# Performance work log

Hardware: AMD Instinct MI355X
Metric: run time of the kernel (lower is better)

Reference implementation:

```python
import jax, jax.numpy as jnp
import numpy as np

B, S, D = 2, 2048, 2048
H = 16
HD = D // H
FF = 8192
EPS = 1e-5


def _layer_norm(x, g, b):
    mu = jnp.mean(x, axis=-1, keepdims=True)
    var = jnp.mean(jnp.square(x - mu), axis=-1, keepdims=True)
    return (x - mu) * jax.lax.rsqrt(var + EPS) * g + b


def setup_inputs() -> dict:
    key = jax.random.key(0)
    ks = jax.random.split(key, 8)
    s = 0.02
    return {
        "x": jax.random.normal(ks[0], (B, S, D), dtype=jnp.float32),
        "ln1_g": jnp.ones((D,), jnp.float32),
        "ln1_b": jnp.zeros((D,), jnp.float32),
        "qkv_w": jax.random.normal(ks[1], (D, 3 * D), dtype=jnp.float32) * s,
        "qkv_b": jnp.zeros((3 * D,), jnp.float32),
        "out_w": jax.random.normal(ks[2], (D, D), dtype=jnp.float32) * s,
        "out_b": jnp.zeros((D,), jnp.float32),
        "ln2_g": jnp.ones((D,), jnp.float32),
        "ln2_b": jnp.zeros((D,), jnp.float32),
        "w1": jax.random.normal(ks[3], (D, FF), dtype=jnp.float32) * s,
        "b1": jnp.zeros((FF,), jnp.float32),
        "w2": jax.random.normal(ks[4], (FF, D), dtype=jnp.float32) * s,
        "b2": jnp.zeros((D,), jnp.float32),
    }


def reference(x, ln1_g, ln1_b, qkv_w, qkv_b, out_w, out_b, ln2_g, ln2_b, w1, b1, w2, b2):
    # --- attention sub-block (pre-norm) ---
    residual = x
    h = _layer_norm(x, ln1_g, ln1_b)
    qkv = h @ qkv_w + qkv_b                      # [B,S,3D]
    q, k, v = jnp.split(qkv, 3, axis=-1)
    # [B,S,D] -> [B,H,S,HD]
    q = q.reshape(B, S, H, HD).transpose(0, 2, 1, 3)
    k = k.reshape(B, S, H, HD).transpose(0, 2, 1, 3)
    v = v.reshape(B, S, H, HD).transpose(0, 2, 1, 3)
    scores = jnp.einsum("bhqd,bhkd->bhqk", q, k)  # [B,H,S,S]
    causal = jnp.triu(jnp.ones((S, S), dtype=bool), k=1)
    scores = jnp.where(causal[None, None], -jnp.inf, scores)
    attn = jax.nn.softmax(scores / np.sqrt(HD).astype(np.float32), axis=-1)
    av = jnp.einsum("bhqk,bhkd->bhqd", attn, v)   # [B,H,S,HD]
    av = av.transpose(0, 2, 1, 3).reshape(B, S, D)
    x = residual + (av @ out_w + out_b)
    # --- FFN sub-block (pre-norm) ---
    residual = x
    h = _layer_norm(x, ln2_g, ln2_b)
    h = jax.nn.gelu(h @ w1 + b1, approximate=False)
    x = residual + (h @ w2 + b2)
    return x
```

## Files before the change

### kernel.cpp

```cpp
#include <hip/hip_runtime.h>
#include <hip/hip_bf16.h>

#define B_  2
#define S_  2048
#define D_  2048
#define H_  16
#define HD_ 128
#define FF_ 8192

typedef __bf16 bf16x8 __attribute__((ext_vector_type(8)));
typedef float  f32x4  __attribute__((ext_vector_type(4)));
typedef unsigned short u16;
typedef u16 u16x8 __attribute__((ext_vector_type(8)));

__device__ __forceinline__ u16 f2bf(float f) {
    union { float f; unsigned u; } c; c.f = f;
    unsigned u = c.u;
    u += 0x7fffu + ((u >> 16) & 1u);
    return (u16)(u >> 16);
}

__device__ __forceinline__ void gld16(void* lds, const void* g) {
    __builtin_amdgcn_global_load_lds(
        (const __attribute__((address_space(1))) unsigned int*)g,
        (__attribute__((address_space(3))) unsigned int*)lds,
        16, 0, 0);
}

__global__ __launch_bounds__(256)
void ln_kernel(const float* __restrict__ x, const float* __restrict__ g,
               const float* __restrict__ bb, u16* __restrict__ out)
{
    int row = blockIdx.x, tid = threadIdx.x;
    const float4* xr = (const float4*)(x + (size_t)row * D_);
    float4 a = xr[tid], c = xr[tid + 256];
    float s  = a.x + a.y + a.z + a.w + c.x + c.y + c.z + c.w;
    float s2 = a.x*a.x + a.y*a.y + a.z*a.z + a.w*a.w
             + c.x*c.x + c.y*c.y + c.z*c.z + c.w*c.w;
    #pragma unroll
    for (int off = 32; off > 0; off >>= 1) {
        s  += __shfl_down(s,  off, 64);
        s2 += __shfl_down(s2, off, 64);
    }
    __shared__ float red[16];
    __shared__ float mr[2];
    int wid = tid >> 6, lane = tid & 63;
    if (lane == 0) { red[wid] = s; red[8 + wid] = s2; }
    __syncthreads();
    if (tid == 0) {
        float ts = red[0] + red[1] + red[2] + red[3];
        float t2 = red[8] + red[9] + red[10] + red[11];
        float mu = ts * (1.0f / D_);
        float var = t2 * (1.0f / D_) - mu * mu;
        mr[0] = mu; mr[1] = rsqrtf(var + 1e-5f);
    }
    __syncthreads();
    float mu = mr[0], rstd = mr[1];
    const float4* gg = (const float4*)g;
    const float4* bv = (const float4*)bb;
    float4 g0 = gg[tid], g1 = gg[tid + 256];
    float4 b0 = bv[tid], b1 = bv[tid + 256];
    u16* orow = out + (size_t)row * D_;
    ushort4 o0, o1;
    o0.x = f2bf((a.x - mu) * rstd * g0.x + b0.x);
    o0.y = f2bf((a.y - mu) * rstd * g0.y + b0.y);
    o0.z = f2bf((a.z - mu) * rstd * g0.z + b0.z);
    o0.w = f2bf((a.w - mu) * rstd * g0.w + b0.w);
    o1.x = f2bf((c.x - mu) * rstd * g1.x + b1.x);
    o1.y = f2bf((c.y - mu) * rstd * g1.y + b1.y);
    o1.z = f2bf((c.z - mu) * rstd * g1.z + b1.z);
    o1.w = f2bf((c.w - mu) * rstd * g1.w + b1.w);
    *(ushort4*)&orow[tid * 4]         = o0;
    *(ushort4*)&orow[(tid + 256) * 4] = o1;
}

__global__ __launch_bounds__(256)
void tcvt_kernel(const float* __restrict__ W, u16* __restrict__ WT, int K, int N)
{
    __shared__ float t[32][33];
    int n0 = blockIdx.x << 5, k0 = blockIdx.y << 5;
    int tx = threadIdx.x & 31, ty = threadIdx.x >> 5;
    #pragma unroll
    for (int i = 0; i < 32; i += 8)
        t[ty + i][tx] = W[(size_t)(k0 + ty + i) * N + n0 + tx];
    __syncthreads();
    #pragma unroll
    for (int i = 0; i < 32; i += 8)
        WT[(size_t)(n0 + ty + i) * K + k0 + tx] = f2bf(t[tx][ty + i]);
}

template<int EPI>
__global__ __launch_bounds__(256)
void gemm_kernel(const u16* __restrict__ A, const u16* __restrict__ BT,
                 const float* __restrict__ bias, const float* __restrict__ res,
                 void* __restrict__ outv, int M, int N, int K)
{
    __shared__ u16 ldsA[128 * 64];
    __shared__ u16 ldsB[128 * 64];
    int tid = threadIdx.x;
    int wid = tid >> 6, lane = tid & 63;
    int wm = wid >> 1, wn = wid & 1;
    int quad = lane >> 4, l16 = lane & 15;

    int tiles_m = M >> 7;
    int bandsz = tiles_m << 4;
    int lin = blockIdx.x;
    int band = lin / bandsz, rr = lin % bandsz;
    int m0 = (rr >> 4) << 7;
    int n0 = ((band << 4) + (rr & 15)) << 7;

    f32x4 acc[4][4] = {};

    int r8 = lane >> 3, c8 = lane & 7;
    int gc = (c8 ^ (r8 & 7)) << 3;
    const u16* pA = A  + (size_t)(m0 + wid * 32 + r8) * K + gc;
    const u16* pB = BT + (size_t)(n0 + wid * 32 + r8) * K + gc;
    u16* lA = ldsA + wid * 32 * 64;
    u16* lB = ldsB + wid * 32 * 64;
    int sw = l16 & 7;

    for (int k0 = 0; k0 < K; k0 += 64) {
        #pragma unroll
        for (int j = 0; j < 4; j++) {
            gld16(lA + j * 512, pA + (size_t)j * 8 * K + k0);
            gld16(lB + j * 512, pB + (size_t)j * 8 * K + k0);
        }
        __syncthreads();
        #pragma unroll
        for (int kk = 0; kk < 2; kk++) {
            bf16x8 af[4], bf[4];
            int co0 = ((kk * 4 + 0) ^ sw) << 3;
            int co1 = ((kk * 4 + 1) ^ sw) << 3;
            int co2 = ((kk * 4 + 2) ^ sw) << 3;
            int co3 = ((kk * 4 + 3) ^ sw) << 3;
            int co = quad == 0 ? co0 : quad == 1 ? co1 : quad == 2 ? co2 : co3;
            #pragma unroll
            for (int t = 0; t < 4; t++) {
                af[t] = *(const bf16x8*)&ldsA[(wm * 64 + t * 16 + l16) * 64 + co];
                bf[t] = *(const bf16x8*)&ldsB[(wn * 64 + t * 16 + l16) * 64 + co];
            }
            #pragma unroll
            for (int i = 0; i < 4; i++)
                #pragma unroll
                for (int j = 0; j < 4; j++)
                    acc[i][j] = __builtin_amdgcn_mfma_f32_16x16x32_bf16(af[i], bf[j], acc[i][j], 0, 0, 0);
        }
        __syncthreads();
    }

    u16*   outb = (u16*)outv;
    float* outf = (float*)outv;
    int colb = n0 + wn * 64, rowb = m0 + wm * 64;
    #pragma unroll
    for (int j = 0; j < 4; j++) {
        int col = colb + j * 16 + l16;
        float bv = bias[col];
        #pragma unroll
        for (int i = 0; i < 4; i++) {
            int row0 = rowb + i * 16 + (quad << 2);
            #pragma unroll
            for (int r = 0; r < 4; r++) {
                float v = acc[i][j][r] + bv;
                size_t idx = (size_t)(row0 + r) * N + col;
                if (EPI == 2) {
                    outf[idx] = v + res[idx];
                } else {
                    if (EPI == 1) v = 0.5f * v * (1.0f + erff(v * 0.70710678118654752f));
                    outb[idx] = f2bf(v);
                }
            }
        }
    }
}

__global__ __launch_bounds__(256, 2)
void attn_kernel(const u16* __restrict__ qkv, u16* __restrict__ av)
{
    __shared__ u16 ldsK[4][64][32];
    __shared__ unsigned ldsVT[128][36];
    __shared__ u16 ldsP[4][32][72];
    int tid = threadIdx.x, wid = tid >> 6, lane = tid & 63;
    int quad = lane >> 4, l16 = lane & 15;
    int bh = blockIdx.y, b = bh >> 4, h = bh & 15;
    int qx = gridDim.x - 1 - blockIdx.x;
    int q0 = qx << 7;
    const u16* base = qkv + (size_t)b * S_ * (3 * D_);

    bf16x8 aq[2][4];
    #pragma unroll
    for (int set = 0; set < 2; set++) {
        int qrow = q0 + set * 64 + wid * 16 + l16;
        const u16* qp = base + (size_t)qrow * (3 * D_) + h * HD_;
        #pragma unroll
        for (int kk = 0; kk < 4; kk++)
            aq[set][kk] = *(const bf16x8*)(qp + kk * 32 + quad * 8);
    }

    float m_i[2][4], l_i[2][4];
    f32x4 oacc[2][8] = {};
    #pragma unroll
    for (int s = 0; s < 2; s++)
        #pragma unroll
        for (int r = 0; r < 4; r++) { m_i[s][r] = -1e30f; l_i[s][r] = 0.f; }

    const float scale = 0.088388347648318447f;
    int ntile = 2 * qx + 2;
    for (int jt = 0; jt < ntile; jt++) {
        int j0 = jt << 6;
        #pragma unroll
        for (int j = 0; j < 4; j++) {
            int c = wid * 4 + j;
            int kk = c >> 2, kb = c & 3;
            int key = (kb << 4) + (lane >> 2);
            const u16* g = base + (size_t)(j0 + key) * (3 * D_) + D_ + h * HD_
                         + kk * 32 + ((lane & 3) << 3);
            gld16((u16*)ldsK + c * 512, g);
        }
        {
            int kp = lane & 31, dhalf = lane >> 5;
            #pragma unroll
            for (int p = 0; p < 2; p++) {
                int doff = wid * 32 + p * 16 + dhalf * 8;
                const u16* g0 = base + (size_t)(j0 + 2 * kp) * (3 * D_)
                              + 2 * D_ + h * HD_ + doff;
                u16x8 v0 = *(const u16x8*)g0;
                u16x8 v1 = *(const u16x8*)(g0 + 3 * D_);
                #pragma unroll
                for (int k = 0; k < 8; k++)
                    ldsVT[doff + k][kp] = (unsigned)v0[k] | ((unsigned)v1[k] << 16);
            }
        }
        __syncthreads();
        f32x4 sacc[2][4] = {};
        #pragma unroll
        for (int kk = 0; kk < 4; kk++)
            #pragma unroll
            for (int n = 0; n < 4; n++) {
                bf16x8 bfr = *(const bf16x8*)&ldsK[kk][(n << 4) + l16][quad << 3];
                sacc[0][n] = __builtin_amdgcn_mfma_f32_16x16x32_bf16(aq[0][kk], bfr, sacc[0][n], 0, 0, 0);
                sacc[1][n] = __builtin_amdgcn_mfma_f32_16x16x32_bf16(aq[1][kk], bfr, sacc[1][n], 0, 0, 0);
            }
        #pragma unroll
        for (int set = 0; set < 2; set++) {
            float rowmax[4] = {-1e30f, -1e30f, -1e30f, -1e30f};
            #pragma unroll
            for (int n = 0; n < 4; n++) {
                int key = j0 + (n << 4) + l16;
                #pragma unroll
                for (int r = 0; r < 4; r++) {
                    float xv = sacc[set][n][r] * scale;
                    int qr = q0 + set * 64 + wid * 16 + (quad << 2) + r;
                    if (key > qr) xv = -1e30f;
                    sacc[set][n][r] = xv;
                    rowmax[r] = fmaxf(rowmax[r], xv);
                }
            }
            #pragma unroll
            for (int off = 1; off < 16; off <<= 1)
                #pragma unroll
                for (int r = 0; r < 4; r++)
                    rowmax[r] = fmaxf(rowmax[r], __shfl_xor(rowmax[r], off, 64));
            float alpha[4], rsum[4];
            #pragma unroll
            for (int r = 0; r < 4; r++) {
                float mn = fmaxf(m_i[set][r], rowmax[r]);
                alpha[r] = __expf(m_i[set][r] - mn);
                m_i[set][r] = mn;
                rsum[r] = 0.f;
            }
            #pragma unroll
            for (int n = 0; n < 4; n++)
                #pragma unroll
                for (int r = 0; r < 4; r++) {
                    float p = __expf(sacc[set][n][r] - m_i[set][r]);
                    rsum[r] += p;
                    ldsP[wid][set * 16 + (quad << 2) + r][(n << 4) + l16] = f2bf(p);
                }
            #pragma unroll
            for (int off = 1; off < 16; off <<= 1)
                #pragma unroll
                for (int r = 0; r < 4; r++)
                    rsum[r] += __shfl_xor(rsum[r], off, 64);
            #pragma unroll
            for (int r = 0; r < 4; r++)
                l_i[set][r] = l_i[set][r] * alpha[r] + rsum[r];
            #pragma unroll
            for (int n = 0; n < 8; n++)
                #pragma unroll
                for (int r = 0; r < 4; r++)
                    oacc[set][n][r] *= alpha[r];
        }
        #pragma unroll
        for (int ks = 0; ks < 2; ks++) {
            bf16x8 pa0 = *(const bf16x8*)&ldsP[wid][l16]     [(ks << 5) + (quad << 3)];
            bf16x8 pa1 = *(const bf16x8*)&ldsP[wid][16 + l16][(ks << 5) + (quad << 3)];
            #pragma unroll
            for (int n = 0; n < 8; n++) {
                bf16x8 vb = *(const bf16x8*)&ldsVT[(n << 4) + l16][(ks << 4) + (quad << 2)];
                oacc[0][n] = __builtin_amdgcn_mfma_f32_16x16x32_bf16(pa0, vb, oacc[0][n], 0, 0, 0);
                oacc[1][n] = __builtin_amdgcn_mfma_f32_16x16x32_bf16(pa1, vb, oacc[1][n], 0, 0, 0);
            }
        }
        __syncthreads();
    }
    #pragma unroll
    for (int set = 0; set < 2; set++)
        #pragma unroll
        for (int r = 0; r < 4; r++) {
            float inv = 1.0f / l_i[set][r];
            int qr = q0 + set * 64 + wid * 16 + (quad << 2) + r;
            u16* op = av + (size_t)(b * S_ + qr) * D_ + h * HD_;
            #pragma unroll
            for (int n = 0; n < 8; n++)
                op[(n << 4) + l16] = f2bf(oacc[set][n][r] * inv);
        }
}

extern "C" void kernel_launch(void* const* d_in, const int* in_sizes, int n_in,
                              void* d_out, int out_size, void* d_ws, size_t ws_size,
                              hipStream_t stream)
{
    const float* x     = (const float*)d_in[0];
    const float* ln1_g = (const float*)d_in[1];
    const float* ln1_b = (const float*)d_in[2];
    const float* qkv_w = (const float*)d_in[3];
    const float* qkv_b = (const float*)d_in[4];
    const float* out_w = (const float*)d_in[5];
    const float* out_b = (const float*)d_in[6];
    const float* ln2_g = (const float*)d_in[7];
    const float* ln2_b = (const float*)d_in[8];
    const float* w1    = (const float*)d_in[9];
    const float* b1    = (const float*)d_in[10];
    const float* w2    = (const float*)d_in[11];
    const float* b2    = (const float*)d_in[12];
    float* out = (float*)d_out;

    char* ws  = (char*)d_ws;
    u16* wT   = (u16*)ws;
    u16* hbuf = (u16*)(ws + (32u << 20));
    u16* big  = (u16*)(ws + (48u << 20));
    u16* qkvb = big;
    u16* ffb  = big;

    dim3 blk(256);

    ln_kernel<<<dim3(B_ * S_), blk, 0, stream>>>(x, ln1_g, ln1_b, hbuf);
    tcvt_kernel<<<dim3(6144 / 32, 2048 / 32), blk, 0, stream>>>(qkv_w, wT, 2048, 6144);
    gemm_kernel<0><<<dim3((6144 / 128) * (4096 / 128)), blk, 0, stream>>>(
        hbuf, wT, qkv_b, nullptr, (void*)qkvb, 4096, 6144, 2048);
    attn_kernel<<<dim3(S_ / 128, B_ * H_), blk, 0, stream>>>(qkvb, hbuf);
    tcvt_kernel<<<dim3(2048 / 32, 2048 / 32), blk, 0, stream>>>(out_w, wT, 2048, 2048);
    gemm_kernel<2><<<dim3((2048 / 128) * (4096 / 128)), blk, 0, stream>>>(
        hbuf, wT, out_b, x, (void*)out, 4096, 2048, 2048);
    ln_kernel<<<dim3(B_ * S_), blk, 0, stream>>>(out, ln2_g, ln2_b, hbuf);
    tcvt_kernel<<<dim3(8192 / 32, 2048 / 32), blk, 0, stream>>>(w1, wT, 2048, 8192);
    gemm_kernel<1><<<dim3((8192 / 128) * (4096 / 128)), blk, 0, stream>>>(
        hbuf, wT, b1, nullptr, (void*)ffb, 4096, 8192, 2048);
    tcvt_kernel<<<dim3(2048 / 32, 8192 / 32), blk, 0, stream>>>(w2, wT, 8192, 2048);
    gemm_kernel<2><<<dim3((2048 / 128) * (4096 / 128)), blk, 0, stream>>>(
        ffb, wT, b2, out, (void*)out, 4096, 2048, 8192);
}
```

Baseline: 931.5 us.

## Rewrite GEMM as 8-wave 128x256 tile with multi-stage pipelined LDS prefetch

The GEMM kernel moves from 4-wave 128x128 tiles with a single-stage load/sync loop to 8-wave 128x256 tiles. It uses double-buffered, half-K-split LDS stages filled by direct global-to-LDS loads, interleaved with MFMA phases under explicit waitcnt, barriers and setprio. A new XCD-aware block swizzle and an LDS read swizzle are added. The goal is to hide global load latency behind MFMA work and improve data reuse, at the cost of much more LDS (about 96KB), fragile hand-counted vmcnt values and register pressure from the 2-blocks-per-CU launch bound.

```diff
diff --git a/kernel.cpp b/kernel.cpp
--- a/kernel.cpp
+++ b/kernel.cpp
@@ -90,62 +90,95 @@
 }
 
 template<int EPI>
-__global__ __launch_bounds__(256)
+__global__ __launch_bounds__(512, 2)
 void gemm_kernel(const u16* __restrict__ A, const u16* __restrict__ BT,
                  const float* __restrict__ bias, const float* __restrict__ res,
                  void* __restrict__ outv, int M, int N, int K)
 {
-    __shared__ u16 ldsA[128 * 64];
-    __shared__ u16 ldsB[128 * 64];
+    __shared__ u16 ldsA[4 * 4096];
+    __shared__ u16 ldsB[4 * 8192];
+    (void)M;
+
     int tid = threadIdx.x;
     int wid = tid >> 6, lane = tid & 63;
-    int wm = wid >> 1, wn = wid & 1;
+    int wm = wid >> 2, wn = wid & 3;
     int quad = lane >> 4, l16 = lane & 15;
 
-    int tiles_m = M >> 7;
-    int bandsz = tiles_m << 4;
-    int lin = blockIdx.x;
-    int band = lin / bandsz, rr = lin % bandsz;
-    int m0 = (rr >> 4) << 7;
-    int n0 = ((band << 4) + (rr & 15)) << 7;
+    int nwg = (int)gridDim.x;
+    int swz = ((int)blockIdx.x & 7) * (nwg >> 3) + ((int)blockIdx.x >> 3);
+    int mt = swz & 31;
+    int nt = swz >> 5;
+    int m0 = mt << 7, n0 = nt << 8;
+
+    int lo3 = (tid & 7) ^ ((tid >> 3) & 7);
+    int rS  = ((tid >> 3) << 1) | (lo3 >> 2);
+    int cS  = (lo3 & 3) << 3;
+    const u16* gA  = A  + (size_t)(m0 + rS) * K + cS;
+    const u16* gB0 = BT + (size_t)(n0 + rS) * K + cS;
+    const u16* gB1 = gB0 + (size_t)128 * K;
+
+    int slot   = (((l16 & 1) << 2) | quad) ^ (l16 >> 1);
+    int laneRd = (l16 >> 1) * 64 + slot * 8;
+    int aRd = wm * 2048 + laneRd;
+    int bRd = wn * 2048 + laneRd;
 
     f32x4 acc[4][4] = {};
-
-    int r8 = lane >> 3, c8 = lane & 7;
-    int gc = (c8 ^ (r8 & 7)) << 3;
-    const u16* pA = A  + (size_t)(m0 + wid * 32 + r8) * K + gc;
-    const u16* pB = BT + (size_t)(n0 + wid * 32 + r8) * K + gc;
-    u16* lA = ldsA + wid * 32 * 64;
-    u16* lB = ldsB + wid * 32 * 64;
-    int sw = l16 & 7;
-
-    for (int k0 = 0; k0 < K; k0 += 64) {
-        #pragma unroll
-        for (int j = 0; j < 4; j++) {
-            gld16(lA + j * 512, pA + (size_t)j * 8 * K + k0);
-            gld16(lB + j * 512, pB + (size_t)j * 8 * K + k0);
-        }
-        __syncthreads();
-        #pragma unroll
-        for (int kk = 0; kk < 2; kk++) {
-            bf16x8 af[4], bf[4];
-            int co0 = ((kk * 4 + 0) ^ sw) << 3;
-            int co1 = ((kk * 4 + 1) ^ sw) << 3;
-            int co2 = ((kk * 4 + 2) ^ sw) << 3;
-            int co3 = ((kk * 4 + 3) ^ sw) << 3;
-            int co = quad == 0 ? co0 : quad == 1 ? co1 : quad == 2 ? co2 : co3;
-            #pragma unroll
-            for (int t = 0; t < 4; t++) {
-                af[t] = *(const bf16x8*)&ldsA[(wm * 64 + t * 16 + l16) * 64 + co];
-                bf[t] = *(const bf16x8*)&ldsB[(wn * 64 + t * 16 + l16) * 64 + co];
-            }
-            #pragma unroll
-            for (int i = 0; i < 4; i++)
-                #pragma unroll
-                for (int j = 0; j < 4; j++)
-                    acc[i][j] = __builtin_amdgcn_mfma_f32_16x16x32_bf16(af[i], bf[j], acc[i][j], 0, 0, 0);
-        }
-        __syncthreads();
+    bf16x8 af[4];
+
+    auto stA = [&](int b, int ks, int kofs) {
+        gld16(ldsA + (b * 2 + ks) * 4096 + wid * 512, gA + kofs);
+    };
+    auto stB = [&](int b, int ks, int kofs) {
+        gld16(ldsB + (b * 2 + ks) * 8192 + wid * 512, gB0 + kofs);
+        gld16(ldsB + (b * 2 + ks) * 8192 + 4096 + wid * 512, gB1 + kofs);
+    };
+    auto phase = [&](int buf, int ks, int nh, bool ar,
+                     bool stb, int sb, int sk, int kofs, bool vm) {
+        if (ar) {
+            #pragma unroll
+            for (int t = 0; t < 4; t++)
+                af[t] = *(const bf16x8*)(ldsA + (buf * 2 + ks) * 4096 + aRd + t * 512);
+        }
+        const u16* bp = ldsB + (buf * 2 + ks) * 8192 + bRd + nh * 1024;
+        bf16x8 bf0 = *(const bf16x8*)bp;
+        bf16x8 bf1 = *(const bf16x8*)(bp + 512);
+        if (!stb) stA(sb, sk, kofs); else stB(sb, sk, kofs);
+        if (vm) asm volatile("s_waitcnt vmcnt(3)" ::: "memory");
+        __builtin_amdgcn_s_barrier();
+        asm volatile("s_waitcnt lgkmcnt(0)" ::: "memory");
+        __builtin_amdgcn_sched_barrier(0);
+        __builtin_amdgcn_s_setprio(1);
+        #pragma unroll
+        for (int i = 0; i < 4; i++) {
+            acc[i][nh * 2 + 0] = __builtin_amdgcn_mfma_f32_16x16x32_bf16(af[i], bf0, acc[i][nh * 2 + 0], 0, 0, 0);
+            acc[i][nh * 2 + 1] = __builtin_amdgcn_mfma_f32_16x16x32_bf16(af[i], bf1, acc[i][nh * 2 + 1], 0, 0, 0);
+        }
+        __builtin_amdgcn_s_setprio(0);
+        __builtin_amdgcn_s_barrier();
+    };
+
+    int nkt = K >> 6;
+    stA(0, 0, 0);  stB(0, 0, 0);
+    stA(0, 1, 32); stB(0, 1, 32);
+    stA(1, 0, 64); stB(1, 0, 64);
+    asm volatile("s_waitcnt vmcnt(3)" ::: "memory");
+    __builtin_amdgcn_s_barrier();
+
+    int niter = nkt >> 1;
+    for (int it = 0; it < niter; ++it) {
+        int t = it << 1;
+        int k1 = ((t + 1) << 6) + 32;
+        int t2 = t + 2; if (t2 > nkt - 1) t2 = nkt - 1;
+        int t3 = t + 3; if (t3 > nkt - 1) t3 = nkt - 1;
+        int k2 = t2 << 6, k3 = t3 << 6;
+        phase(0, 0, 0, true,  false, 1, 1, k1,      false);
+        phase(0, 0, 1, false, true,  1, 1, k1,      false);
+        phase(0, 1, 0, true,  false, 0, 0, k2,      false);
+        phase(0, 1, 1, false, true,  0, 0, k2,      true);
+        phase(1, 0, 0, true,  false, 0, 1, k2 + 32, false);
+        phase(1, 0, 1, false, true,  0, 1, k2 + 32, false);
+        phase(1, 1, 0, true,  false, 1, 0, k3,      false);
+        phase(1, 1, 1, false, true,  1, 0, k3,      true);
     }
 
     u16*   outb = (u16*)outv;
@@ -343,20 +376,21 @@
     u16* ffb  = big;
 
     dim3 blk(256);
+    dim3 gblk(512);
 
     ln_kernel<<<dim3(B_ * S_), blk, 0, stream>>>(x, ln1_g, ln1_b, hbuf);
     tcvt_kernel<<<dim3(6144 / 32, 2048 / 32), blk, 0, stream>>>(qkv_w, wT, 2048, 6144);
-    gemm_kernel<0><<<dim3((6144 / 128) * (4096 / 128)), blk, 0, stream>>>(
+    gemm_kernel<0><<<dim3((6144 / 256) * (4096 / 128)), gblk, 0, stream>>>(
         hbuf, wT, qkv_b, nullptr, (void*)qkvb, 4096, 6144, 2048);
     attn_kernel<<<dim3(S_ / 128, B_ * H_), blk, 0, stream>>>(qkvb, hbuf);
     tcvt_kernel<<<dim3(2048 / 32, 2048 / 32), blk, 0, stream>>>(out_w, wT, 2048, 2048);
-    gemm_kernel<2><<<dim3((2048 / 128) * (4096 / 128)), blk, 0, stream>>>(
+    gemm_kernel<2><<<dim3((2048 / 256) * (4096 / 128)), gblk, 0, stream>>>(
         hbuf, wT, out_b, x, (void*)out, 4096, 2048, 2048);
     ln_kernel<<<dim3(B_ * S_), blk, 0, stream>>>(out, ln2_g, ln2_b, hbuf);
     tcvt_kernel<<<dim3(8192 / 32, 2048 / 32), blk, 0, stream>>>(w1, wT, 2048, 8192);
-    gemm_kernel<1><<<dim3((8192 / 128) * (4096 / 128)), blk, 0, stream>>>(
+    gemm_kernel<1><<<dim3((8192 / 256) * (4096 / 128)), gblk, 0, stream>>>(
         hbuf, wT, b1, nullptr, (void*)ffb, 4096, 8192, 2048);
     tcvt_kernel<<<dim3(2048 / 32, 8192 / 32), blk, 0, stream>>>(w2, wT, 8192, 2048);
-    gemm_kernel<2><<<dim3((2048 / 128) * (4096 / 128)), blk, 0, stream>>>(
+    gemm_kernel<2><<<dim3((2048 / 256) * (4096 / 128)), gblk, 0, stream>>>(
         ffb, wT, b2, out, (void*)out, 4096, 2048, 8192);
 }
```

Result: slower. 1.039 ms (+11.6%).
